# Kernel optimization log

Hardware: AMD Instinct MI355X
Metric: run time of the kernel (lower is better)

Reference implementation:

```python
import jax, jax.numpy as jnp
import numpy as np

NUM_BUCKETS = 64
MAX_DISTANCE = 50000.0


def setup_inputs() -> dict:
    R, I, N, E, H = 64, 512, 4, 256, 8
    key = jax.random.key(0)
    ks = jax.random.split(key, 12)
    p = lambda k, shape: (jax.random.normal(k, shape, dtype=jnp.float32) * 0.02)
    return {
        "x": jax.random.normal(ks[0], (R, I, N, E), dtype=jnp.float32),
        "distances": jax.random.randint(ks[1], (N, I, I), 0, 50000).astype(jnp.int32),
        "Wq": p(ks[2], (E, E)), "bq": jnp.zeros((E,), jnp.float32),
        "Wk": p(ks[3], (E, E)), "bk": jnp.zeros((E,), jnp.float32),
        "Wv": p(ks[4], (E, E)), "bv": jnp.zeros((E,), jnp.float32),
        "Wo": p(ks[5], (E, E)), "bo": jnp.zeros((E,), jnp.float32),
        "rel_emb": p(ks[6], (NUM_BUCKETS, H)),
    }


def reference(x, distances, Wq, bq, Wk, bk, Wv, bv, Wo, bo, rel_emb):
    R, I, N, E = x.shape
    H = rel_emb.shape[1]
    D = E // H
    # scaling = head_dim**-0.5 / sqrt(num_rows)
    scaling = (D ** -0.5) / np.sqrt(R)

    def proj(W, b):
        return (jnp.einsum('rine,fe->rinf', x, W) + b).reshape(R, I, N, H, D)

    q = proj(Wq, bq) * scaling
    k = proj(Wk, bk)
    v = proj(Wv, bv)

    # Row-summed attention logits: (H, N, I, J)
    attn_weights = jnp.einsum('rinhd,rjnhd->hnij', q, k)

    # T5-style relative position bias (buckets = linspace boundaries)
    buckets = jnp.linspace(0.0, MAX_DISTANCE, NUM_BUCKETS - 1)
    abs_dist = jnp.abs(distances).astype(jnp.float32)
    # torch.bucketize(right=False) == searchsorted side='left'
    bucket_idx = jnp.searchsorted(buckets, abs_dist, side='left')  # (N, I, J)
    bias = rel_emb[bucket_idx]                  # (N, I, J, H)
    attn_weights = attn_weights + jnp.transpose(bias, (3, 0, 1, 2))

    attn_probs = jax.nn.softmax(attn_weights, axis=-1)  # dropout p=0.0 -> identity

    context = jnp.einsum('hnij,rjnhd->rinhd', attn_probs, v).reshape(R, I, N, E)
    output = jnp.einsum('rine,fe->rinf', context, Wo) + bo
    return output, attn_probs
```

## Files before the change

kernel.cpp:

```cpp
#include <hip/hip_runtime.h>

typedef unsigned short u16;
typedef unsigned int u32;
typedef float f32x4 __attribute__((ext_vector_type(4)));
typedef short bf16x8 __attribute__((ext_vector_type(8)));
typedef unsigned short u16x8 __attribute__((ext_vector_type(8)));

#define SL 33554432u

__device__ __forceinline__ float bf2f(u16 u) {
  u32 v = ((u32)u) << 16;
  return __builtin_bit_cast(float, v);
}
__device__ __forceinline__ u16 f2bf(float f) {
  u32 i = __builtin_bit_cast(u32, f);
  i += 0x7fffu + ((i >> 16) & 1u);
  return (u16)(i >> 16);
}

#define GLDS16(g, l) __builtin_amdgcn_global_load_lds( \
    (const __attribute__((address_space(1))) void*)(g), \
    (__attribute__((address_space(3))) void*)(l), 16, 0, 0)

__device__ __forceinline__ void stage128(const u16* gbase, int ldk, u16* lds, int tid) {
  #pragma unroll
  for (int rep = 0; rep < 4; ++rep) {
    int c = tid + rep * 256;
    int row = c >> 3, slot = c & 7;
    const u16* g = gbase + (size_t)row * ldk + ((slot ^ (row & 7)) << 3);
    GLDS16(g, lds + c * 8);
  }
}

__device__ __forceinline__ void mfma128(const u16* As, const u16* Bs, int lane,
                                        int wm0, int wn0, f32x4 acc[4][4]) {
  #pragma unroll
  for (int kk = 0; kk < 2; ++kk) {
    bf16x8 a[4], b[4];
    #pragma unroll
    for (int mi = 0; mi < 4; ++mi) {
      int r = wm0 + mi * 16 + (lane & 15);
      int c16 = (kk * 4 + (lane >> 4)) ^ (r & 7);
      a[mi] = *(const bf16x8*)(As + r * 64 + c16 * 8);
    }
    #pragma unroll
    for (int ni = 0; ni < 4; ++ni) {
      int r = wn0 + ni * 16 + (lane & 15);
      int c16 = (kk * 4 + (lane >> 4)) ^ (r & 7);
      b[ni] = *(const bf16x8*)(Bs + r * 64 + c16 * 8);
    }
    #pragma unroll
    for (int mi = 0; mi < 4; ++mi)
      #pragma unroll
      for (int ni = 0; ni < 4; ++ni)
        acc[mi][ni] = __builtin_amdgcn_mfma_f32_16x16x32_bf16(a[mi], b[ni], acc[mi][ni], 0, 0, 0);
  }
}

__device__ __forceinline__ void gemm_core(const u16* A, int ldkA, const u16* B, int ldkB,
                                          int NT, u16* As, u16* Bs,
                                          int tid, int lane, int wm0, int wn0,
                                          f32x4 acc[4][4]) {
  for (int t = 0; t < NT; ++t) {
    stage128(A + t * 64, ldkA, As, tid);
    stage128(B + t * 64, ldkB, Bs, tid);
    __syncthreads();
    mfma128(As, Bs, lane, wm0, wn0, acc);
    __syncthreads();
  }
}

__global__ __launch_bounds__(256) void k_cast(const float* __restrict__ src,
                                              u16* __restrict__ dst, int n8) {
  int idx = blockIdx.x * 256 + threadIdx.x;
  if (idx >= n8) return;
  const float4* s = (const float4*)src;
  float4 a = s[(size_t)idx * 2], b = s[(size_t)idx * 2 + 1];
  u16x8 o;
  o[0] = f2bf(a.x); o[1] = f2bf(a.y); o[2] = f2bf(a.z); o[3] = f2bf(a.w);
  o[4] = f2bf(b.x); o[5] = f2bf(b.y); o[6] = f2bf(b.z); o[7] = f2bf(b.w);
  *(u16x8*)(dst + (size_t)idx * 8) = o;
}

__global__ __launch_bounds__(256) void k_proj_mm(
    const u16* __restrict__ xb, const u16* __restrict__ Wb,
    const float* __restrict__ bq, const float* __restrict__ bk, const float* __restrict__ bv,
    u16* __restrict__ qt, u16* __restrict__ kt, u16* __restrict__ vt, float scaling) {
  __shared__ __align__(16) u16 As[128 * 64];
  __shared__ __align__(16) u16 Bs[128 * 64];
  const int tid = threadIdx.x, lane = tid & 63, wave = tid >> 6;
  const int wm0 = (wave >> 1) * 64, wn0 = (wave & 1) * 64;
  const int w = blockIdx.z;
  const int m0 = blockIdx.x * 128, n0 = blockIdx.y * 128;

  f32x4 acc[4][4];
  #pragma unroll
  for (int mi = 0; mi < 4; ++mi)
    #pragma unroll
    for (int ni = 0; ni < 4; ++ni) acc[mi][ni] = (f32x4){0.f, 0.f, 0.f, 0.f};

  gemm_core(xb + (size_t)m0 * 256, 256, Wb + w * 65536 + (size_t)n0 * 256, 256,
            4, As, Bs, tid, lane, wm0, wn0, acc);

  const float* bias = (w == 0) ? bq : (w == 1) ? bk : bv;
  u16* dst = (w == 0) ? qt : (w == 1) ? kt : vt;
  const float sc = (w == 0) ? scaling : 1.0f;

  #pragma unroll
  for (int mi = 0; mi < 4; ++mi)
    #pragma unroll
    for (int ni = 0; ni < 4; ++ni) {
      int f = n0 + wn0 + ni * 16 + (lane & 15);
      int h = f >> 5, d = f & 31;
      float bb = bias[f];
      #pragma unroll
      for (int q = 0; q < 4; ++q) {
        int m = m0 + wm0 + mi * 16 + (lane >> 4) * 4 + q;
        int n = m & 3, i = (m >> 2) & 511, r = m >> 11;
        size_t o = ((size_t)((n * 8 + h) * 512 + i)) * 2048 + r * 32 + d;
        dst[o] = f2bf((acc[mi][ni][q] + bb) * sc);
      }
    }
}

__global__ __launch_bounds__(256) void k_attn_mm(
    const u16* __restrict__ qt, const u16* __restrict__ kt, u16* __restrict__ lgt) {
  __shared__ __align__(16) u16 As[128 * 64];
  __shared__ __align__(16) u16 Bs[128 * 64];
  const int tid = threadIdx.x, lane = tid & 63, wave = tid >> 6;
  const int wm0 = (wave >> 1) * 64, wn0 = (wave & 1) * 64;
  const int nh = blockIdx.y;
  const int m0 = (blockIdx.x >> 2) * 128, n0 = (blockIdx.x & 3) * 128;

  f32x4 acc[4][4];
  #pragma unroll
  for (int mi = 0; mi < 4; ++mi)
    #pragma unroll
    for (int ni = 0; ni < 4; ++ni) acc[mi][ni] = (f32x4){0.f, 0.f, 0.f, 0.f};

  const size_t base = (size_t)nh * 512 * 2048;
  gemm_core(qt + base + (size_t)m0 * 2048, 2048, kt + base + (size_t)n0 * 2048, 2048,
            32, As, Bs, tid, lane, wm0, wn0, acc);

  #pragma unroll
  for (int mi = 0; mi < 4; ++mi)
    #pragma unroll
    for (int ni = 0; ni < 4; ++ni) {
      int col = n0 + wn0 + ni * 16 + (lane & 15);
      #pragma unroll
      for (int q = 0; q < 4; ++q) {
        int row = m0 + wm0 + mi * 16 + (lane >> 4) * 4 + q;
        lgt[(size_t)nh * 262144 + (size_t)row * 512 + col] = f2bf(acc[mi][ni][q]);
      }
    }
}

__global__ __launch_bounds__(256) void k_softmax(
    const u16* __restrict__ lgt, const int* __restrict__ dist, const float* __restrict__ rel,
    float* __restrict__ probs, u16* __restrict__ pbf) {
  __shared__ float wred[8];
  const int t = threadIdx.x;
  const int b = blockIdx.x;
  const int it = b & 63, h = (b >> 6) & 7, n = b >> 9;
  const int i0 = it * 8, nh = n * 8 + h;

  for (int g = 0; g < 8; ++g) {
    const int i = i0 + g;
    const size_t lrow = ((size_t)nh * 512 + i) * 512;
    float v1 = bf2f(lgt[lrow + t]);
    float v2 = bf2f(lgt[lrow + t + 256]);
    int d1 = dist[((size_t)n * 512 + i) * 512 + t];
    int d2 = dist[((size_t)n * 512 + i) * 512 + t + 256];
    d1 = d1 < 0 ? -d1 : d1;  d2 = d2 < 0 ? -d2 : d2;
    int u1 = (62 * d1 + 49999) / 50000; if (u1 > 63) u1 = 63;
    int u2 = (62 * d2 + 49999) / 50000; if (u2 > 63) u2 = 63;
    v1 += rel[u1 * 8 + h];
    v2 += rel[u2 * 8 + h];

    float m = fmaxf(v1, v2);
    #pragma unroll
    for (int off = 32; off; off >>= 1) m = fmaxf(m, __shfl_xor(m, off));
    if ((t & 63) == 0) wred[t >> 6] = m;
    __syncthreads();
    m = fmaxf(fmaxf(wred[0], wred[1]), fmaxf(wred[2], wred[3]));
    float e1 = __expf(v1 - m), e2 = __expf(v2 - m);
    float s = e1 + e2;
    #pragma unroll
    for (int off = 32; off; off >>= 1) s += __shfl_xor(s, off);
    if ((t & 63) == 0) wred[4 + (t >> 6)] = s;
    __syncthreads();
    s = (wred[4] + wred[5]) + (wred[6] + wred[7]);
    float inv = 1.0f / s;
    float p1 = e1 * inv, p2 = e2 * inv;
    size_t po = ((size_t)(h * 4 + n) * 512 + i) * 512;
    probs[po + t] = p1;
    probs[po + t + 256] = p2;
    size_t pb = ((size_t)nh * 512 + i) * 512;
    pbf[pb + t] = f2bf(p1);
    pbf[pb + t + 256] = f2bf(p2);
    __syncthreads();
  }
}

__global__ __launch_bounds__(256) void k_vtrans(const u16* __restrict__ vt, u16* __restrict__ vtt) {
  __shared__ u16 ts[64][72];
  const int b = blockIdx.x;
  const int ct_ = b & 31, it = (b >> 5) & 7, nh = b >> 8;
  const int i0 = it * 64, c0 = ct_ * 64;
  const int t = threadIdx.x;
  #pragma unroll
  for (int rep = 0; rep < 2; ++rep) {
    int c = t + rep * 256;
    int r = c >> 3, q = c & 7;
    u16x8 v = *(const u16x8*)(vt + ((size_t)nh * 512 + i0 + r) * 2048 + c0 + q * 8);
    #pragma unroll
    for (int j = 0; j < 8; ++j) ts[r][q * 8 + j] = v[j];
  }
  __syncthreads();
  #pragma unroll
  for (int rep = 0; rep < 2; ++rep) {
    int c = t + rep * 256;
    int rr = c >> 3, q = c & 7;
    u16x8 o;
    #pragma unroll
    for (int j = 0; j < 8; ++j) o[j] = ts[q * 8 + j][rr];
    *(u16x8*)(vtt + ((size_t)nh * 2048 + c0 + rr) * 512 + i0 + q * 8) = o;
  }
}

__global__ __launch_bounds__(256) void k_ctx_mm(
    const u16* __restrict__ vtt, const u16* __restrict__ pbf, u16* __restrict__ ctT) {
  __shared__ __align__(16) u16 As[128 * 64];
  __shared__ __align__(16) u16 Bs[128 * 64];
  const int tid = threadIdx.x, lane = tid & 63, wave = tid >> 6;
  const int wm0 = (wave >> 1) * 64, wn0 = (wave & 1) * 64;
  const int nh = blockIdx.y;
  const int m0 = (blockIdx.x >> 2) * 128, n0 = (blockIdx.x & 3) * 128;

  f32x4 acc[4][4];
  #pragma unroll
  for (int mi = 0; mi < 4; ++mi)
    #pragma unroll
    for (int ni = 0; ni < 4; ++ni) acc[mi][ni] = (f32x4){0.f, 0.f, 0.f, 0.f};

  gemm_core(vtt + (size_t)nh * 1048576 + (size_t)m0 * 512, 512,
            pbf + (size_t)nh * 262144 + (size_t)n0 * 512, 512,
            8, As, Bs, tid, lane, wm0, wn0, acc);

  #pragma unroll
  for (int mi = 0; mi < 4; ++mi)
    #pragma unroll
    for (int ni = 0; ni < 4; ++ni) {
      int col = n0 + wn0 + ni * 16 + (lane & 15);
      #pragma unroll
      for (int q = 0; q < 4; ++q) {
        int row = m0 + wm0 + mi * 16 + (lane >> 4) * 4 + q;
        ctT[(size_t)nh * 1048576 + (size_t)row * 512 + col] = f2bf(acc[mi][ni][q]);
      }
    }
}

__global__ __launch_bounds__(256) void k_ctrans(const u16* __restrict__ ctT, u16* __restrict__ ct) {
  __shared__ u16 ts[32][520];
  const int b = blockIdx.x;
  const int r = b & 63, nh = b >> 6;
  const int n = nh >> 3, h = nh & 7;
  const int t = threadIdx.x;
  #pragma unroll
  for (int rep = 0; rep < 8; ++rep) {
    int c = t + rep * 256;
    int d = c >> 6, q = c & 63;
    u16x8 v = *(const u16x8*)(ctT + ((size_t)nh * 2048 + r * 32 + d) * 512 + q * 8);
    #pragma unroll
    for (int j = 0; j < 8; ++j) ts[d][q * 8 + j] = v[j];
  }
  __syncthreads();
  #pragma unroll
  for (int rep = 0; rep < 8; ++rep) {
    int c = t + rep * 256;
    int i = c >> 2, q = c & 3;
    u16x8 o;
    #pragma unroll
    for (int j = 0; j < 8; ++j) o[j] = ts[q * 8 + j][i];
    *(u16x8*)(ct + ((size_t)((r * 512 + i) * 4 + n)) * 256 + h * 32 + q * 8) = o;
  }
}

__global__ __launch_bounds__(256) void k_oproj_mm(
    const u16* __restrict__ ct, const u16* __restrict__ Wob,
    const float* __restrict__ bo, float* __restrict__ out) {
  __shared__ __align__(16) u16 As[128 * 64];
  __shared__ __align__(16) u16 Bs[128 * 64];
  const int tid = threadIdx.x, lane = tid & 63, wave = tid >> 6;
  const int wm0 = (wave >> 1) * 64, wn0 = (wave & 1) * 64;
  const int m0 = (blockIdx.x >> 1) * 128, n0 = (blockIdx.x & 1) * 128;

  f32x4 acc[4][4];
  #pragma unroll
  for (int mi = 0; mi < 4; ++mi)
    #pragma unroll
    for (int ni = 0; ni < 4; ++ni) acc[mi][ni] = (f32x4){0.f, 0.f, 0.f, 0.f};

  gemm_core(ct + (size_t)m0 * 256, 256, Wob + (size_t)n0 * 256, 256,
            4, As, Bs, tid, lane, wm0, wn0, acc);

  #pragma unroll
  for (int mi = 0; mi < 4; ++mi)
    #pragma unroll
    for (int ni = 0; ni < 4; ++ni) {
      int col = n0 + wn0 + ni * 16 + (lane & 15);
      float bb = bo[col];
      #pragma unroll
      for (int q = 0; q < 4; ++q) {
        int row = m0 + wm0 + mi * 16 + (lane >> 4) * 4 + q;
        out[(size_t)row * 256 + col] = acc[mi][ni][q] + bb;
      }
    }
}

extern "C" void kernel_launch(void* const* d_in, const int* in_sizes, int n_in,
                              void* d_out, int out_size, void* d_ws, size_t ws_size,
                              hipStream_t stream) {
  const float* x  = (const float*)d_in[0];
  const int* dist = (const int*)d_in[1];
  const float* Wq = (const float*)d_in[2];
  const float* bq = (const float*)d_in[3];
  const float* Wk = (const float*)d_in[4];
  const float* bk = (const float*)d_in[5];
  const float* Wv = (const float*)d_in[6];
  const float* bv = (const float*)d_in[7];
  const float* Wo = (const float*)d_in[8];
  const float* bo = (const float*)d_in[9];
  const float* rel = (const float*)d_in[10];
  float* out = (float*)d_out;
  float* probs = out + (size_t)SL;

  u16* ws = (u16*)d_ws;
  u16* xb  = ws;
  u16* qt  = ws + (size_t)SL;
  u16* kt  = ws + (size_t)2 * SL;
  u16* vt  = ws + (size_t)3 * SL;
  u16* lgt = xb;
  u16* pbf = qt;
  u16* vtt = kt;
  u16* ctT = vt;
  u16* ctb = xb;
  u16* Wb  = ws + (size_t)4 * SL;

  const float scaling = 0.022097086912079608f;

  k_cast<<<16384, 256, 0, stream>>>(x, xb, 4194304);
  k_cast<<<32, 256, 0, stream>>>(Wq, Wb, 8192);
  k_cast<<<32, 256, 0, stream>>>(Wk, Wb + 65536, 8192);
  k_cast<<<32, 256, 0, stream>>>(Wv, Wb + 131072, 8192);
  k_cast<<<32, 256, 0, stream>>>(Wo, Wb + 196608, 8192);

  k_proj_mm<<<dim3(1024, 2, 3), 256, 0, stream>>>(xb, Wb, bq, bk, bv, qt, kt, vt, scaling);
  k_attn_mm<<<dim3(16, 32), 256, 0, stream>>>(qt, kt, lgt);
  k_softmax<<<2048, 256, 0, stream>>>(lgt, dist, rel, probs, pbf);
  k_vtrans<<<8192, 256, 0, stream>>>(vt, vtt);
  k_ctx_mm<<<dim3(64, 32), 256, 0, stream>>>(vtt, pbf, ctT);
  k_ctrans<<<2048, 256, 0, stream>>>(ctT, ctb);
  k_oproj_mm<<<2048, 256, 0, stream>>>(ctb, Wb + 196608, bo, out);
}
```

Baseline: 391.6 us.

## Fuse x cast into projection, batch weight casts, XCD-swizzle grids, vectorize softmax

The fp32-to-bf16 cast of x is folded into the projection GEMM's A-tile staging, removing a full bf16 copy of x through global memory. The four weight casts become one launch. The GEMM grids are flattened and block IDs remapped so that consecutive tiles land on the same XCD for L2 reuse. Softmax is rewritten to one row per wavefront with 8-wide vector loads and stores, wave-only reductions and no block syncs, reusing the bucketed distances across two heads. The cost is that the projection now loads fp32 x through registers instead of the async global-to-LDS path, which raises A-tile traffic per block and stalls the MFMA loop.

```diff
diff --git a/kernel.cpp b/kernel.cpp
--- a/kernel.cpp
+++ b/kernel.cpp
@@ -29,6 +29,20 @@
     int row = c >> 3, slot = c & 7;
     const u16* g = gbase + (size_t)row * ldk + ((slot ^ (row & 7)) << 3);
     GLDS16(g, lds + c * 8);
+  }
+}
+
+__device__ __forceinline__ void stage128_f32(const float* gbase, int ldk, u16* lds, int tid) {
+  #pragma unroll
+  for (int rep = 0; rep < 4; ++rep) {
+    int c = tid + rep * 256;
+    int row = c >> 3, slot = c & 7;
+    const float* g = gbase + (size_t)row * ldk + ((slot ^ (row & 7)) << 3);
+    float4 a = *(const float4*)g, b = *(const float4*)(g + 4);
+    u16x8 o;
+    o[0] = f2bf(a.x); o[1] = f2bf(a.y); o[2] = f2bf(a.z); o[3] = f2bf(a.w);
+    o[4] = f2bf(b.x); o[5] = f2bf(b.y); o[6] = f2bf(b.z); o[7] = f2bf(b.w);
+    *(u16x8*)(lds + c * 8) = o;
   }
 }
 
@@ -70,28 +84,33 @@
   }
 }
 
-__global__ __launch_bounds__(256) void k_cast(const float* __restrict__ src,
-                                              u16* __restrict__ dst, int n8) {
+__global__ __launch_bounds__(256) void k_castw(
+    const float* __restrict__ Wq, const float* __restrict__ Wk,
+    const float* __restrict__ Wv, const float* __restrict__ Wo,
+    u16* __restrict__ Wb) {
   int idx = blockIdx.x * 256 + threadIdx.x;
-  if (idx >= n8) return;
-  const float4* s = (const float4*)src;
-  float4 a = s[(size_t)idx * 2], b = s[(size_t)idx * 2 + 1];
+  int w = idx >> 13, off = idx & 8191;
+  const float* src = (w == 0) ? Wq : (w == 1) ? Wk : (w == 2) ? Wv : Wo;
+  const float4* s = (const float4*)(src + (size_t)off * 8);
+  float4 a = s[0], b = s[1];
   u16x8 o;
   o[0] = f2bf(a.x); o[1] = f2bf(a.y); o[2] = f2bf(a.z); o[3] = f2bf(a.w);
   o[4] = f2bf(b.x); o[5] = f2bf(b.y); o[6] = f2bf(b.z); o[7] = f2bf(b.w);
-  *(u16x8*)(dst + (size_t)idx * 8) = o;
+  *(u16x8*)(Wb + (size_t)w * 65536 + (size_t)off * 8) = o;
 }
 
 __global__ __launch_bounds__(256) void k_proj_mm(
-    const u16* __restrict__ xb, const u16* __restrict__ Wb,
+    const float* __restrict__ x, const u16* __restrict__ Wb,
     const float* __restrict__ bq, const float* __restrict__ bk, const float* __restrict__ bv,
     u16* __restrict__ qt, u16* __restrict__ kt, u16* __restrict__ vt, float scaling) {
   __shared__ __align__(16) u16 As[128 * 64];
   __shared__ __align__(16) u16 Bs[128 * 64];
   const int tid = threadIdx.x, lane = tid & 63, wave = tid >> 6;
   const int wm0 = (wave >> 1) * 64, wn0 = (wave & 1) * 64;
-  const int w = blockIdx.z;
-  const int m0 = blockIdx.x * 128, n0 = blockIdx.y * 128;
+  const int bid = blockIdx.x;
+  const int sb = (bid & 7) * 768 + (bid >> 3);
+  const int mt = sb / 6, g = sb % 6;
+  const int m0 = mt * 128, n0 = (g & 1) * 128, w = g >> 1;
 
   f32x4 acc[4][4];
   #pragma unroll
@@ -99,8 +118,15 @@
     #pragma unroll
     for (int ni = 0; ni < 4; ++ni) acc[mi][ni] = (f32x4){0.f, 0.f, 0.f, 0.f};
 
-  gemm_core(xb + (size_t)m0 * 256, 256, Wb + w * 65536 + (size_t)n0 * 256, 256,
-            4, As, Bs, tid, lane, wm0, wn0, acc);
+  const float* Ax = x + (size_t)m0 * 256;
+  const u16* Bw = Wb + w * 65536 + (size_t)n0 * 256;
+  for (int t = 0; t < 4; ++t) {
+    stage128_f32(Ax + t * 64, 256, As, tid);
+    stage128(Bw + t * 64, 256, Bs, tid);
+    __syncthreads();
+    mfma128(As, Bs, lane, wm0, wn0, acc);
+    __syncthreads();
+  }
 
   const float* bias = (w == 0) ? bq : (w == 1) ? bk : bv;
   u16* dst = (w == 0) ? qt : (w == 1) ? kt : vt;
@@ -129,8 +155,10 @@
   __shared__ __align__(16) u16 Bs[128 * 64];
   const int tid = threadIdx.x, lane = tid & 63, wave = tid >> 6;
   const int wm0 = (wave >> 1) * 64, wn0 = (wave & 1) * 64;
-  const int nh = blockIdx.y;
-  const int m0 = (blockIdx.x >> 2) * 128, n0 = (blockIdx.x & 3) * 128;
+  const int bid = blockIdx.x;
+  const int sb = (bid & 7) * 64 + (bid >> 3);
+  const int nh = sb >> 4, tt = sb & 15;
+  const int m0 = (tt >> 2) * 128, n0 = (tt & 3) * 128;
 
   f32x4 acc[4][4];
   #pragma unroll
@@ -158,47 +186,54 @@
 __global__ __launch_bounds__(256) void k_softmax(
     const u16* __restrict__ lgt, const int* __restrict__ dist, const float* __restrict__ rel,
     float* __restrict__ probs, u16* __restrict__ pbf) {
-  __shared__ float wred[8];
   const int t = threadIdx.x;
+  const int lane = t & 63, wv = t >> 6;
   const int b = blockIdx.x;
-  const int it = b & 63, h = (b >> 6) & 7, n = b >> 9;
-  const int i0 = it * 8, nh = n * 8 + h;
-
-  for (int g = 0; g < 8; ++g) {
-    const int i = i0 + g;
-    const size_t lrow = ((size_t)nh * 512 + i) * 512;
-    float v1 = bf2f(lgt[lrow + t]);
-    float v2 = bf2f(lgt[lrow + t + 256]);
-    int d1 = dist[((size_t)n * 512 + i) * 512 + t];
-    int d2 = dist[((size_t)n * 512 + i) * 512 + t + 256];
-    d1 = d1 < 0 ? -d1 : d1;  d2 = d2 < 0 ? -d2 : d2;
-    int u1 = (62 * d1 + 49999) / 50000; if (u1 > 63) u1 = 63;
-    int u2 = (62 * d2 + 49999) / 50000; if (u2 > 63) u2 = 63;
-    v1 += rel[u1 * 8 + h];
-    v2 += rel[u2 * 8 + h];
-
-    float m = fmaxf(v1, v2);
-    #pragma unroll
-    for (int off = 32; off; off >>= 1) m = fmaxf(m, __shfl_xor(m, off));
-    if ((t & 63) == 0) wred[t >> 6] = m;
-    __syncthreads();
-    m = fmaxf(fmaxf(wred[0], wred[1]), fmaxf(wred[2], wred[3]));
-    float e1 = __expf(v1 - m), e2 = __expf(v2 - m);
-    float s = e1 + e2;
+  const int i = b & 511, n = b >> 9;
+
+  const int* dr = dist + ((size_t)n * 512 + i) * 512 + lane * 8;
+  int4 dA = *(const int4*)dr, dB = *(const int4*)(dr + 4);
+  int dd[8] = {dA.x, dA.y, dA.z, dA.w, dB.x, dB.y, dB.z, dB.w};
+  int u[8];
+  #pragma unroll
+  for (int j = 0; j < 8; ++j) {
+    int v = dd[j] < 0 ? -dd[j] : dd[j];
+    int q = (62 * v + 49999) / 50000; if (q > 63) q = 63;
+    u[j] = q;
+  }
+
+  #pragma unroll
+  for (int hh = 0; hh < 2; ++hh) {
+    const int h = wv * 2 + hh;
+    const int nh = n * 8 + h;
+    const u16* lr = lgt + ((size_t)nh * 512 + i) * 512 + lane * 8;
+    u16x8 L = *(const u16x8*)lr;
+    float vj[8];
+    float mx = -1e30f;
+    #pragma unroll
+    for (int j = 0; j < 8; ++j) {
+      vj[j] = bf2f(L[j]) + rel[u[j] * 8 + h];
+      mx = fmaxf(mx, vj[j]);
+    }
+    #pragma unroll
+    for (int off = 32; off; off >>= 1) mx = fmaxf(mx, __shfl_xor(mx, off));
+    float s = 0.f;
+    #pragma unroll
+    for (int j = 0; j < 8; ++j) { vj[j] = __expf(vj[j] - mx); s += vj[j]; }
     #pragma unroll
     for (int off = 32; off; off >>= 1) s += __shfl_xor(s, off);
-    if ((t & 63) == 0) wred[4 + (t >> 6)] = s;
-    __syncthreads();
-    s = (wred[4] + wred[5]) + (wred[6] + wred[7]);
     float inv = 1.0f / s;
-    float p1 = e1 * inv, p2 = e2 * inv;
-    size_t po = ((size_t)(h * 4 + n) * 512 + i) * 512;
-    probs[po + t] = p1;
-    probs[po + t + 256] = p2;
-    size_t pb = ((size_t)nh * 512 + i) * 512;
-    pbf[pb + t] = f2bf(p1);
-    pbf[pb + t + 256] = f2bf(p2);
-    __syncthreads();
+    float4 pa, pb;
+    pa.x = vj[0]*inv; pa.y = vj[1]*inv; pa.z = vj[2]*inv; pa.w = vj[3]*inv;
+    pb.x = vj[4]*inv; pb.y = vj[5]*inv; pb.z = vj[6]*inv; pb.w = vj[7]*inv;
+    size_t po = ((size_t)(h * 4 + n) * 512 + i) * 512 + lane * 8;
+    *(float4*)(probs + po) = pa;
+    *(float4*)(probs + po + 4) = pb;
+    u16x8 pc;
+    pc[0]=f2bf(pa.x); pc[1]=f2bf(pa.y); pc[2]=f2bf(pa.z); pc[3]=f2bf(pa.w);
+    pc[4]=f2bf(pb.x); pc[5]=f2bf(pb.y); pc[6]=f2bf(pb.z); pc[7]=f2bf(pb.w);
+    size_t pq = ((size_t)nh * 512 + i) * 512 + lane * 8;
+    *(u16x8*)(pbf + pq) = pc;
   }
 }
 
@@ -234,8 +269,10 @@
   __shared__ __align__(16) u16 Bs[128 * 64];
   const int tid = threadIdx.x, lane = tid & 63, wave = tid >> 6;
   const int wm0 = (wave >> 1) * 64, wn0 = (wave & 1) * 64;
-  const int nh = blockIdx.y;
-  const int m0 = (blockIdx.x >> 2) * 128, n0 = (blockIdx.x & 3) * 128;
+  const int bid = blockIdx.x;
+  const int sb = (bid & 7) * 256 + (bid >> 3);
+  const int nh = sb >> 6, tt = sb & 63;
+  const int m0 = (tt >> 2) * 128, n0 = (tt & 3) * 128;
 
   f32x4 acc[4][4];
   #pragma unroll
@@ -293,7 +330,9 @@
   __shared__ __align__(16) u16 Bs[128 * 64];
   const int tid = threadIdx.x, lane = tid & 63, wave = tid >> 6;
   const int wm0 = (wave >> 1) * 64, wn0 = (wave & 1) * 64;
-  const int m0 = (blockIdx.x >> 1) * 128, n0 = (blockIdx.x & 1) * 128;
+  const int bid = blockIdx.x;
+  const int sb = (bid & 7) * 256 + (bid >> 3);
+  const int m0 = (sb >> 1) * 128, n0 = (sb & 1) * 128;
 
   f32x4 acc[4][4];
   #pragma unroll
@@ -336,30 +375,24 @@
   float* probs = out + (size_t)SL;
 
   u16* ws = (u16*)d_ws;
-  u16* xb  = ws;
+  u16* lgt = ws;
   u16* qt  = ws + (size_t)SL;
   u16* kt  = ws + (size_t)2 * SL;
   u16* vt  = ws + (size_t)3 * SL;
-  u16* lgt = xb;
   u16* pbf = qt;
   u16* vtt = kt;
   u16* ctT = vt;
-  u16* ctb = xb;
+  u16* ctb = lgt;
   u16* Wb  = ws + (size_t)4 * SL;
 
   const float scaling = 0.022097086912079608f;
 
-  k_cast<<<16384, 256, 0, stream>>>(x, xb, 4194304);
-  k_cast<<<32, 256, 0, stream>>>(Wq, Wb, 8192);
-  k_cast<<<32, 256, 0, stream>>>(Wk, Wb + 65536, 8192);
-  k_cast<<<32, 256, 0, stream>>>(Wv, Wb + 131072, 8192);
-  k_cast<<<32, 256, 0, stream>>>(Wo, Wb + 196608, 8192);
-
-  k_proj_mm<<<dim3(1024, 2, 3), 256, 0, stream>>>(xb, Wb, bq, bk, bv, qt, kt, vt, scaling);
-  k_attn_mm<<<dim3(16, 32), 256, 0, stream>>>(qt, kt, lgt);
+  k_castw  <<<128, 256, 0, stream>>>(Wq, Wk, Wv, Wo, Wb);
+  k_proj_mm<<<6144, 256, 0, stream>>>(x, Wb, bq, bk, bv, qt, kt, vt, scaling);
+  k_attn_mm<<<512, 256, 0, stream>>>(qt, kt, lgt);
   k_softmax<<<2048, 256, 0, stream>>>(lgt, dist, rel, probs, pbf);
-  k_vtrans<<<8192, 256, 0, stream>>>(vt, vtt);
-  k_ctx_mm<<<dim3(64, 32), 256, 0, stream>>>(vtt, pbf, ctT);
-  k_ctrans<<<2048, 256, 0, stream>>>(ctT, ctb);
+  k_vtrans <<<8192, 256, 0, stream>>>(vt, vtt);
+  k_ctx_mm <<<2048, 256, 0, stream>>>(vtt, pbf, ctT);
+  k_ctrans <<<2048, 256, 0, stream>>>(ctT, ctb);
   k_oproj_mm<<<2048, 256, 0, stream>>>(ctb, Wb + 196608, bo, out);
 }
```

After: 402.0 us. 2.7% more time.
